# Optimization experiments

Measured on AMD Instinct MI355X. Metric: run time of the kernel, lower is better.

The kernel has to match this reference:

```python
import jax, jax.numpy as jnp
import numpy as np

B, N, T, N_IN = 8, 64, 128, 8
N_EMB = 64
E = N * (N - 1)  # fully connected, no self loops


def _rel_matrices():
    off_diag = np.ones((N, N), dtype=np.float32) - np.eye(N, dtype=np.float32)
    recv_idx, send_idx = np.where(off_diag)
    rel_rec = np.eye(N, dtype=np.float32)[recv_idx]   # [E, N]
    rel_send = np.eye(N, dtype=np.float32)[send_idx]  # [E, N]
    return jnp.asarray(rel_rec), jnp.asarray(rel_send)


def setup_inputs() -> dict:
    key = jax.random.key(0)
    ks = jax.random.split(key, 8)
    x = jax.random.normal(ks[0], (B, N, T, N_IN), dtype=jnp.float32)
    rel_rec, rel_send = _rel_matrices()
    s = lambda fan_in: 1.0 / np.sqrt(fan_in)
    W_sp = jax.random.uniform(ks[1], (3 * N_IN, N_EMB), minval=-s(3 * N_IN), maxval=s(3 * N_IN))
    b_sp = jax.random.uniform(ks[2], (N_EMB,), minval=-s(3 * N_IN), maxval=s(3 * N_IN))
    W_node = jax.random.uniform(ks[3], (N_IN, N_EMB), minval=-s(N_IN), maxval=s(N_IN))
    b_node = jax.random.uniform(ks[4], (N_EMB,), minval=-s(N_IN), maxval=s(N_IN))
    W_att = jax.random.uniform(ks[5], (N_EMB, 1), minval=-s(N_EMB), maxval=s(N_EMB))
    b_att = jax.random.uniform(ks[6], (1,), minval=-s(N_EMB), maxval=s(N_EMB))
    return {"x": x, "rel_rec": rel_rec, "rel_send": rel_send,
            "W_sp": W_sp, "b_sp": b_sp, "W_node": W_node, "b_node": b_node,
            "W_att": W_att, "b_att": b_att}


def reference(x, rel_rec, rel_send, W_sp, b_sp, W_node, b_node, W_att, b_att):
    lrelu = jax.nn.leaky_relu  # slope 0.01, matches F.leaky_relu default

    # gather senders per edge: [B, E, T, F]
    senders = jnp.einsum('en,bntf->betf', rel_send, x)
    # NOTE: faithful to source bug: receivers = senders.view(...) overwrites
    receivers = senders
    spatial_relations = receivers - senders  # zeros, as in the original

    nodes_embed = x @ W_node + b_node  # [B, N, T, D]

    # model_increment=True branch
    xd = x[:, :, 1:, :] - x[:, :, :-1, :]  # [B, N, T-1, F]
    senders = jnp.einsum('en,bntf->betf', rel_send, xd)
    receivers = senders  # same bug replicated
    rec_send = jnp.concatenate([senders, receivers], axis=-1)  # [B, E, T-1, 2F]
    spatial_relations = jnp.concatenate(
        [spatial_relations[:, :, :-1, :], rec_send], axis=-1)  # [B, E, T-1, 3F]
    nodes_embed = nodes_embed[:, :, :-1, :]  # [B, N, T-1, D]

    spatial_embed = spatial_relations @ W_sp + b_sp  # [B, E, T-1, D]

    nodes_embed = jnp.transpose(nodes_embed, (0, 2, 1, 3))    # [B, T-1, N, D]
    spatial_embed = jnp.transpose(spatial_embed, (0, 2, 1, 3))  # [B, T-1, E, D]

    receivers_embed = jnp.einsum('en,btnd->bted', rel_rec, nodes_embed)
    senders_embed = jnp.einsum('en,btnd->bted', rel_send, nodes_embed)
    agg = receivers_embed + senders_embed + spatial_embed  # [B, T-1, E, D]

    attention = lrelu((agg @ W_att + b_att)[..., 0])  # [B, T-1, E]
    # rel_rec.T @ diag(attention) @ rel_send, without materializing [E, E]
    A = jnp.einsum('en,bte,ef->btnf', rel_rec, attention, rel_send)  # [B,T-1,N,N]
    A = jax.nn.softmax(A, axis=-1)
    return lrelu(A @ nodes_embed)  # [B, T-1, N, D]
```

## Files before the change

### kernel.cpp

```cpp
#include <hip/hip_runtime.h>
#include <math.h>

#define BB 8
#define TM1 127

typedef _Float16 f16x4 __attribute__((ext_vector_type(4)));
typedef float f32x4 __attribute__((ext_vector_type(4)));
typedef unsigned int u32x4 __attribute__((ext_vector_type(4)));

__device__ __forceinline__ float lrelu(float v) { return v > 0.0f ? v : 0.01f * v; }

__global__ __launch_bounds__(256, 4) void gat_kernel(
    const float* __restrict__ x,
    const float* __restrict__ W_sp,
    const float* __restrict__ b_sp,
    const float* __restrict__ W_node,
    const float* __restrict__ b_node,
    const float* __restrict__ W_att,
    const float* __restrict__ b_att,
    float* __restrict__ out)
{
    const int bt = blockIdx.x;
    const int b = bt / TM1;
    const int t = bt - b * TM1;
    const int tid = threadIdx.x;
    const int lane = tid & 63;
    const int wid = tid >> 6;

    __shared__ __align__(16) unsigned short Nh[64][72];
    __shared__ __align__(16) float u_sh[64];
    __shared__ __align__(16) float w_sh[64];
    __shared__ __align__(16) float red[20];

    const float wa = W_att[lane];
    float Wn[8];
#pragma unroll
    for (int k = 0; k < 8; ++k) Wn[k] = W_node[k * 64 + lane];
    const float bnode_d = b_node[lane];
    const float batt = b_att[0];

    f32x4 xa0, xa1, xd0, xd1;
    if (wid == 0) {
        const float* xr = x + ((b * 64 + lane) * 128 + t) * 8;
        xa0 = *(const f32x4*)(xr);
        xa1 = *(const f32x4*)(xr + 4);
        xd0 = *(const f32x4*)(xr + 8);
        xd1 = *(const f32x4*)(xr + 12);
    }

    {
        const int v0 = wid * 5;
        float pr[5];
#pragma unroll
        for (int j = 0; j < 5; ++j) {
            int v = v0 + j;
            float val;
            if (v < 8)       val = W_node[v * 64 + lane] * wa;
            else if (v < 16) val = (W_sp[v * 64 + lane] + W_sp[(v + 8) * 64 + lane]) * wa;
            else if (v == 16) val = b_sp[lane] * wa;
            else             val = bnode_d * wa;
            pr[j] = val;
        }
#pragma unroll
        for (int j = 0; j < 5; ++j) {
            float vv = pr[j];
#pragma unroll
            for (int off = 1; off < 64; off <<= 1) vv += __shfl_xor(vv, off, 64);
            pr[j] = vv;
        }
        if (lane == 0) {
#pragma unroll
            for (int j = 0; j < 5; ++j) {
                int v = v0 + j;
                if (v < 18) red[v] = pr[j];
            }
        }
    }

    {
        unsigned int hw[8];
#pragma unroll
        for (int p = 0; p < 8; ++p) {
            int f0 = wid * 16 + 2 * p;
            int off = ((b * 64 + f0) * 128 + t) * 8;
            off = __builtin_amdgcn_readfirstlane(off);
            const float* r0 = x + off;
            const float* r1 = r0 + 1024;
            float acc0 = bnode_d, acc1 = bnode_d;
#pragma unroll
            for (int e = 0; e < 8; ++e) {
                acc0 += r0[e] * Wn[e];
                acc1 += r1[e] * Wn[e];
            }
            _Float16 h0 = (_Float16)acc0, h1 = (_Float16)acc1;
            hw[p] = (unsigned int)__builtin_bit_cast(unsigned short, h0) |
                    ((unsigned int)__builtin_bit_cast(unsigned short, h1) << 16);
        }
        u32x4 qa = {hw[0], hw[1], hw[2], hw[3]};
        u32x4 qb = {hw[4], hw[5], hw[6], hw[7]};
        *(u32x4*)&Nh[lane][wid * 16]     = qa;
        *(u32x4*)&Nh[lane][wid * 16 + 8] = qb;
    }
    __syncthreads();

    if (wid == 0) {
        float su = 0.f, sw = 0.f;
#pragma unroll
        for (int e = 0; e < 4; ++e) {
            su += xa0[e] * red[e] + xa1[e] * red[4 + e];
            sw += (xd0[e] - xa0[e]) * red[8 + e] + (xd1[e] - xa1[e]) * red[12 + e];
        }
        u_sh[lane] = su + red[17];
        w_sh[lane] = sw + red[16];
    }
    __syncthreads();

    {
        const int i = lane & 15;
        const int g4 = (lane >> 4) * 4;
        const int n = wid * 16 + i;
        const float un = u_sh[n];

        float a[16];
#pragma unroll
        for (int s4 = 0; s4 < 4; ++s4) {
            f32x4 uf = *(const f32x4*)&u_sh[s4 * 16 + g4];
            f32x4 wf = *(const f32x4*)&w_sh[s4 * 16 + g4];
#pragma unroll
            for (int e = 0; e < 4; ++e) {
                int f = s4 * 16 + g4 + e;
                float v = lrelu(un + uf[e] + wf[e] + batt);
                a[s4 * 4 + e] = (f == n) ? 0.0f : v;
            }
        }
        float m = a[0];
#pragma unroll
        for (int j = 1; j < 16; ++j) m = fmaxf(m, a[j]);
        m = fmaxf(m, __shfl_xor(m, 16, 64));
        m = fmaxf(m, __shfl_xor(m, 32, 64));
        float s = 0.f;
#pragma unroll
        for (int j = 0; j < 16; ++j) {
            float e = __expf(a[j] - m);
            a[j] = e;
            s += e;
        }
        s += __shfl_xor(s, 16, 64);
        s += __shfl_xor(s, 32, 64);
        const float inv = 1.0f / s;

        f16x4 Ah[4];
#pragma unroll
        for (int s4 = 0; s4 < 4; ++s4)
#pragma unroll
            for (int e = 0; e < 4; ++e)
                Ah[s4][e] = (_Float16)(a[s4 * 4 + e] * inv);

        f32x4 acc[4];
#pragma unroll
        for (int c = 0; c < 4; ++c) acc[c] = (f32x4){0.f, 0.f, 0.f, 0.f};

#pragma unroll
        for (int c = 0; c < 4; ++c) {
            const int col = c * 16 + i;
#pragma unroll
            for (int s4 = 0; s4 < 4; ++s4) {
                f16x4 bh = *(const f16x4*)&Nh[col][s4 * 16 + g4];
                acc[c] = __builtin_amdgcn_mfma_f32_16x16x16f16(Ah[s4], bh, acc[c], 0, 0, 0);
            }
        }

        float* op = out + ((long)(b * TM1 + t) << 12);
#pragma unroll
        for (int c = 0; c < 4; ++c) {
#pragma unroll
            for (int r = 0; r < 4; ++r) {
                int row = wid * 16 + g4 + r;
                op[row * 64 + c * 16 + i] = lrelu(acc[c][r]);
            }
        }
    }
}

extern "C" void kernel_launch(void* const* d_in, const int* in_sizes, int n_in,
                              void* d_out, int out_size, void* d_ws, size_t ws_size,
                              hipStream_t stream) {
    const float* x      = (const float*)d_in[0];
    const float* W_sp   = (const float*)d_in[3];
    const float* b_sp   = (const float*)d_in[4];
    const float* W_node = (const float*)d_in[5];
    const float* b_node = (const float*)d_in[6];
    const float* W_att  = (const float*)d_in[7];
    const float* b_att  = (const float*)d_in[8];
    float* out = (float*)d_out;

    dim3 grid(BB * TM1);
    dim3 block(256);
    hipLaunchKernelGGL(gat_kernel, grid, block, 0, stream,
                       x, W_sp, b_sp, W_node, b_node, W_att, b_att, out);
}
```

Measured before the change: 14.69 us.

## Compute node embeddings with MFMA in registers, drop LDS staging and fold bias

Each wave now computes the full 64x64 node embedding with 16x16x16 f16 MFMAs. It pads the K=8 input dimension to 16 with zeros. The result is kept in registers in exactly the B-operand layout needed by the attention-times-embedding MFMA, which removes the LDS array, its stores and reads, and the scalar FMA loop. Because softmax rows sum to one, the node bias is added after the second MFMA instead of into the embedding. The attention logit terms are also pre-combined into a single shared array. The cost is four-fold redundant embedding work across waves, and x and W_node are now rounded to fp16 before the first product.

```diff
diff --git a/kernel.cpp b/kernel.cpp
--- a/kernel.cpp
+++ b/kernel.cpp
@@ -1,14 +1,12 @@
 #include <hip/hip_runtime.h>
 #include <math.h>
 
-#define BB 8
 #define TM1 127
 
 typedef _Float16 f16x4 __attribute__((ext_vector_type(4)));
 typedef float f32x4 __attribute__((ext_vector_type(4)));
-typedef unsigned int u32x4 __attribute__((ext_vector_type(4)));
-
-__device__ __forceinline__ float lrelu(float v) { return v > 0.0f ? v : 0.01f * v; }
+
+__device__ __forceinline__ float lrelu(float v) { return fmaxf(v, 0.01f * v); }
 
 __global__ __launch_bounds__(256, 4) void gat_kernel(
     const float* __restrict__ x,
@@ -26,18 +24,15 @@
     const int tid = threadIdx.x;
     const int lane = tid & 63;
     const int wid = tid >> 6;
-
-    __shared__ __align__(16) unsigned short Nh[64][72];
+    const int i = lane & 15;
+    const int g = lane >> 4;
+    const int g4 = g * 4;
+
     __shared__ __align__(16) float u_sh[64];
-    __shared__ __align__(16) float w_sh[64];
-    __shared__ __align__(16) float red[20];
+    __shared__ __align__(16) float v_sh[64];
+    __shared__ float red[20];
 
     const float wa = W_att[lane];
-    float Wn[8];
-#pragma unroll
-    for (int k = 0; k < 8; ++k) Wn[k] = W_node[k * 64 + lane];
-    const float bnode_d = b_node[lane];
-    const float batt = b_att[0];
 
     f32x4 xa0, xa1, xd0, xd1;
     if (wid == 0) {
@@ -48,6 +43,34 @@
         xd1 = *(const f32x4*)(xr + 12);
     }
 
+    f16x4 xf[4], wf[4];
+    if (g < 2) {
+#pragma unroll
+        for (int s4 = 0; s4 < 4; ++s4) {
+            const float* p = x + ((b * 64 + s4 * 16 + i) * 128 + t) * 8 + g4;
+            f32x4 v = *(const f32x4*)p;
+            f16x4 h;
+#pragma unroll
+            for (int e = 0; e < 4; ++e) h[e] = (_Float16)v[e];
+            xf[s4] = h;
+        }
+#pragma unroll
+        for (int c = 0; c < 4; ++c) {
+            f16x4 h;
+#pragma unroll
+            for (int e = 0; e < 4; ++e) h[e] = (_Float16)W_node[(g4 + e) * 64 + c * 16 + i];
+            wf[c] = h;
+        }
+    } else {
+#pragma unroll
+        for (int s4 = 0; s4 < 4; ++s4) {
+            f16x4 z;
+#pragma unroll
+            for (int e = 0; e < 4; ++e) z[e] = (_Float16)0.0f;
+            xf[s4] = z; wf[s4] = z;
+        }
+    }
+
     {
         const int v0 = wid * 5;
         float pr[5];
@@ -55,10 +78,10 @@
         for (int j = 0; j < 5; ++j) {
             int v = v0 + j;
             float val;
-            if (v < 8)       val = W_node[v * 64 + lane] * wa;
-            else if (v < 16) val = (W_sp[v * 64 + lane] + W_sp[(v + 8) * 64 + lane]) * wa;
+            if (v < 8)        val = W_node[v * 64 + lane] * wa;
+            else if (v < 16)  val = (W_sp[v * 64 + lane] + W_sp[(v + 8) * 64 + lane]) * wa;
             else if (v == 16) val = b_sp[lane] * wa;
-            else             val = bnode_d * wa;
+            else              val = b_node[lane] * wa;
             pr[j] = val;
         }
 #pragma unroll
@@ -77,29 +100,18 @@
         }
     }
 
-    {
-        unsigned int hw[8];
-#pragma unroll
-        for (int p = 0; p < 8; ++p) {
-            int f0 = wid * 16 + 2 * p;
-            int off = ((b * 64 + f0) * 128 + t) * 8;
-            off = __builtin_amdgcn_readfirstlane(off);
-            const float* r0 = x + off;
-            const float* r1 = r0 + 1024;
-            float acc0 = bnode_d, acc1 = bnode_d;
-#pragma unroll
-            for (int e = 0; e < 8; ++e) {
-                acc0 += r0[e] * Wn[e];
-                acc1 += r1[e] * Wn[e];
-            }
-            _Float16 h0 = (_Float16)acc0, h1 = (_Float16)acc1;
-            hw[p] = (unsigned int)__builtin_bit_cast(unsigned short, h0) |
-                    ((unsigned int)__builtin_bit_cast(unsigned short, h1) << 16);
-        }
-        u32x4 qa = {hw[0], hw[1], hw[2], hw[3]};
-        u32x4 qb = {hw[4], hw[5], hw[6], hw[7]};
-        *(u32x4*)&Nh[lane][wid * 16]     = qa;
-        *(u32x4*)&Nh[lane][wid * 16 + 8] = qb;
+    f16x4 B16[4][4];
+#pragma unroll
+    for (int c = 0; c < 4; ++c) {
+#pragma unroll
+        for (int s4 = 0; s4 < 4; ++s4) {
+            f32x4 d = __builtin_amdgcn_mfma_f32_16x16x16f16(
+                xf[s4], wf[c], (f32x4){0.f, 0.f, 0.f, 0.f}, 0, 0, 0);
+            f16x4 h;
+#pragma unroll
+            for (int e = 0; e < 4; ++e) h[e] = (_Float16)d[e];
+            B16[c][s4] = h;
+        }
     }
     __syncthreads();
 
@@ -110,27 +122,25 @@
             su += xa0[e] * red[e] + xa1[e] * red[4 + e];
             sw += (xd0[e] - xa0[e]) * red[8 + e] + (xd1[e] - xa1[e]) * red[12 + e];
         }
-        u_sh[lane] = su + red[17];
-        w_sh[lane] = sw + red[16];
+        float u = su + red[17];
+        u_sh[lane] = u;
+        v_sh[lane] = u + sw + red[16] + b_att[0];
     }
     __syncthreads();
 
     {
-        const int i = lane & 15;
-        const int g4 = (lane >> 4) * 4;
         const int n = wid * 16 + i;
         const float un = u_sh[n];
 
         float a[16];
 #pragma unroll
         for (int s4 = 0; s4 < 4; ++s4) {
-            f32x4 uf = *(const f32x4*)&u_sh[s4 * 16 + g4];
-            f32x4 wf = *(const f32x4*)&w_sh[s4 * 16 + g4];
+            f32x4 vf = *(const f32x4*)&v_sh[s4 * 16 + g4];
 #pragma unroll
             for (int e = 0; e < 4; ++e) {
-                int f = s4 * 16 + g4 + e;
-                float v = lrelu(un + uf[e] + wf[e] + batt);
-                a[s4 * 4 + e] = (f == n) ? 0.0f : v;
+                float q = un + vf[e];
+                float v = lrelu(q);
+                a[s4 * 4 + e] = (s4 * 16 + g4 + e == n) ? 0.0f : v;
             }
         }
         float m = a[0];
@@ -159,16 +169,15 @@
         f32x4 acc[4];
 #pragma unroll
         for (int c = 0; c < 4; ++c) acc[c] = (f32x4){0.f, 0.f, 0.f, 0.f};
-
-#pragma unroll
-        for (int c = 0; c < 4; ++c) {
-            const int col = c * 16 + i;
-#pragma unroll
-            for (int s4 = 0; s4 < 4; ++s4) {
-                f16x4 bh = *(const f16x4*)&Nh[col][s4 * 16 + g4];
-                acc[c] = __builtin_amdgcn_mfma_f32_16x16x16f16(Ah[s4], bh, acc[c], 0, 0, 0);
-            }
-        }
+#pragma unroll
+        for (int c = 0; c < 4; ++c)
+#pragma unroll
+            for (int s4 = 0; s4 < 4; ++s4)
+                acc[c] = __builtin_amdgcn_mfma_f32_16x16x16f16(Ah[s4], B16[c][s4], acc[c], 0, 0, 0);
+
+        float bn[4];
+#pragma unroll
+        for (int c = 0; c < 4; ++c) bn[c] = b_node[c * 16 + i];
 
         float* op = out + ((long)(b * TM1 + t) << 12);
 #pragma unroll
@@ -176,7 +185,7 @@
 #pragma unroll
             for (int r = 0; r < 4; ++r) {
                 int row = wid * 16 + g4 + r;
-                op[row * 64 + c * 16 + i] = lrelu(acc[c][r]);
+                op[row * 64 + c * 16 + i] = lrelu(acc[c][r] + bn[c]);
             }
         }
     }
@@ -194,7 +203,7 @@
     const float* b_att  = (const float*)d_in[8];
     float* out = (float*)d_out;
 
-    dim3 grid(BB * TM1);
+    dim3 grid(8 * TM1);
     dim3 block(256);
     hipLaunchKernelGGL(gat_kernel, grid, block, 0, stream,
                        x, W_sp, b_sp, W_node, b_node, W_att, b_att, out);
```

Result: no change. 14.80 us (median of 2 runs) (+0.7%).
